# Kernel optimization log

Hardware: AMD Instinct MI355X
Metric: run time of the kernel (lower is better)

Reference implementation:

```python
import jax, jax.numpy as jnp
import numpy as np

D_MODEL, D_HEAD, N_HEADS, N_KV_HEADS = 4096, 128, 32, 8
EPS = 1e-5
N = 2048


def rms_norm(x, w, eps):
    return x * jax.lax.rsqrt(jnp.mean(x * x, axis=-1, keepdims=True) + eps) * w


def rope_swap(x):
    # [x0, x1, x2, x3] -> [-x1, x0, -x3, x2]
    xp = x.reshape(x.shape[:-1] + (-1, 2))
    return jnp.stack([-xp[..., 1], xp[..., 0]], axis=-1).reshape(x.shape)


def rope_rotate(x, r_cos, r_sin):
    return x * r_cos + rope_swap(x) * r_sin


def setup_inputs() -> dict:
    key = jax.random.key(0)
    ks = jax.random.split(key, 8)
    sd = 1.0 / np.sqrt(D_MODEL)
    return {
        "x": jax.random.normal(ks[0], (N, D_MODEL), dtype=jnp.float32),
        "r_cos": jax.random.normal(ks[1], (N, D_HEAD), dtype=jnp.float32),
        "r_sin": jax.random.normal(ks[2], (N, D_HEAD), dtype=jnp.float32),
        "w_norm": jnp.ones((D_MODEL,), dtype=jnp.float32),
        "wq": jax.random.normal(ks[3], (D_MODEL, N_HEADS * D_HEAD), dtype=jnp.float32) * sd,
        "wk": jax.random.normal(ks[4], (D_MODEL, N_KV_HEADS * D_HEAD), dtype=jnp.float32) * sd,
        "wv": jax.random.normal(ks[5], (D_MODEL, N_KV_HEADS * D_HEAD), dtype=jnp.float32) * sd,
        "wo": jax.random.normal(ks[6], (D_MODEL, D_MODEL), dtype=jnp.float32) * sd,
    }


def reference(x, r_cos, r_sin, w_norm, wq, wk, wv, wo):
    n = x.shape[0]
    residual = x
    h = rms_norm(x, w_norm, EPS)

    # projections -> [n_heads, n, d_head]
    q = (h @ wq).reshape(n, N_HEADS, D_HEAD).transpose(1, 0, 2)
    k = (h @ wk).reshape(n, N_KV_HEADS, D_HEAD).transpose(1, 0, 2)
    v = (h @ wv).reshape(n, N_KV_HEADS, D_HEAD).transpose(1, 0, 2)

    # GQA: repeat kv heads
    reps = N_HEADS // N_KV_HEADS
    k = jnp.repeat(k, reps, axis=0)
    v = jnp.repeat(v, reps, axis=0)

    q = rope_rotate(q, r_cos, r_sin)
    k = rope_rotate(k, r_cos, r_sin)

    mask = jnp.where(
        jnp.tril(jnp.ones((n, n), dtype=bool)), 0.0, -jnp.inf
    ).astype(x.dtype)
    scores = jnp.einsum("hnd,hmd->hnm", q, k) / np.sqrt(D_HEAD).astype(np.float32) + mask
    a = jnp.einsum("hnm,hmd->hnd", jax.nn.softmax(scores, axis=-1), v)

    a = a.transpose(1, 0, 2).reshape(n, N_HEADS * D_HEAD)
    return residual + a @ wo
```

## Files before the change

kernel.cpp:

```cpp
#include <hip/hip_runtime.h>
#include <stdint.h>
#include <math.h>

#define TOK 2048
#define DMODEL 4096
#define QKV_LD 5120
#define KVB 64
#define PS_LD 72

typedef __attribute__((ext_vector_type(8))) short short8;
typedef __attribute__((ext_vector_type(4))) short short4v;
typedef __attribute__((ext_vector_type(8))) __bf16 bf16x8;
typedef __attribute__((ext_vector_type(4))) float f32x4;

__device__ __forceinline__ unsigned short f2bf(float f) {
  unsigned u = __float_as_uint(f);
  u += 0x7fffu + ((u >> 16) & 1u);
  return (unsigned short)(u >> 16);
}

__device__ __forceinline__ void gl16(const void* g, void* l) {
  __builtin_amdgcn_global_load_lds((__attribute__((address_space(1))) void*)g,
                                   (__attribute__((address_space(3))) void*)l,
                                   16, 0, 0);
}

__device__ __forceinline__ f32x4 mfma16(short8 a, short8 b, f32x4 c) {
  return __builtin_amdgcn_mfma_f32_16x16x32_bf16(__builtin_bit_cast(bf16x8, a),
                                                 __builtin_bit_cast(bf16x8, b),
                                                 c, 0, 0, 0);
}

__device__ __forceinline__ float fexp2(float x) {
  float r;
  asm("v_exp_f32 %0, %1" : "=v"(r) : "v"(x));
  return r;
}

__global__ __launch_bounds__(256) void k_rmsnorm(const float* __restrict__ x,
                                                 const float* __restrict__ w,
                                                 unsigned short* __restrict__ h) {
  const int row = blockIdx.x;
  const float* xr = x + (size_t)row * DMODEL;
  float4 v[4];
  float ss = 0.f;
#pragma unroll
  for (int i = 0; i < 4; ++i) {
    v[i] = *(const float4*)(xr + threadIdx.x * 4 + i * 1024);
    ss += v[i].x * v[i].x + v[i].y * v[i].y + v[i].z * v[i].z + v[i].w * v[i].w;
  }
#pragma unroll
  for (int m = 1; m < 64; m <<= 1) ss += __shfl_xor(ss, m, 64);
  __shared__ float ws4[4];
  if ((threadIdx.x & 63) == 0) ws4[threadIdx.x >> 6] = ss;
  __syncthreads();
  const float scale = rsqrtf((ws4[0] + ws4[1] + ws4[2] + ws4[3]) * (1.0f / DMODEL) + 1e-5f);
  unsigned short* hr = h + (size_t)row * DMODEL;
#pragma unroll
  for (int i = 0; i < 4; ++i) {
    int col = threadIdx.x * 4 + i * 1024;
    float4 wv = *(const float4*)(w + col);
    uint2 o;
    o.x = (unsigned)f2bf(v[i].x * scale * wv.x) | ((unsigned)f2bf(v[i].y * scale * wv.y) << 16);
    o.y = (unsigned)f2bf(v[i].z * scale * wv.z) | ((unsigned)f2bf(v[i].w * scale * wv.w) << 16);
    *(uint2*)(hr + col) = o;
  }
}

__global__ __launch_bounds__(256) void k_wconvert(const float* __restrict__ W,
                                                  unsigned short* __restrict__ WT,
                                                  int K, int N) {
  __shared__ unsigned short tile[64][65];
  const int n0 = blockIdx.x * 64, k0 = blockIdx.y * 64;
  const int t = threadIdx.x;
  {
    const int r = t >> 2, c0 = (t & 3) * 16;
    const float* src = W + (size_t)(k0 + r) * N + n0 + c0;
#pragma unroll
    for (int i = 0; i < 4; ++i) {
      float4 f = *(const float4*)(src + i * 4);
      tile[r][c0 + i * 4 + 0] = f2bf(f.x);
      tile[r][c0 + i * 4 + 1] = f2bf(f.y);
      tile[r][c0 + i * 4 + 2] = f2bf(f.z);
      tile[r][c0 + i * 4 + 3] = f2bf(f.w);
    }
  }
  __syncthreads();
  {
    const int n = t >> 2, c0 = (t & 3) * 16;
    unsigned short* dst = WT + (size_t)(n0 + n) * K + k0 + c0;
    unsigned short v[16];
#pragma unroll
    for (int i = 0; i < 16; ++i) v[i] = tile[c0 + i][n];
    uint4 o0, o1;
    o0.x = v[0] | ((unsigned)v[1] << 16);  o0.y = v[2] | ((unsigned)v[3] << 16);
    o0.z = v[4] | ((unsigned)v[5] << 16);  o0.w = v[6] | ((unsigned)v[7] << 16);
    o1.x = v[8] | ((unsigned)v[9] << 16);  o1.y = v[10] | ((unsigned)v[11] << 16);
    o1.z = v[12] | ((unsigned)v[13] << 16); o1.w = v[14] | ((unsigned)v[15] << 16);
    *(uint4*)dst = o0;
    *(uint4*)(dst + 8) = o1;
  }
}

__device__ __forceinline__ short8 rdfrag(const unsigned short* buf, int row, int kc) {
  return *(const short8*)((const char*)buf + row * 128 + ((kc ^ (row & 7)) << 4));
}

template <int BM, int BN, int HALF>
__device__ __forceinline__ void stage_half(const unsigned short* __restrict__ A,
                                           const unsigned short* __restrict__ BT,
                                           unsigned short* __restrict__ buf,
                                           int m0, int n0, int K, int kt, int tid) {
  constexpr int AL = BM / 64, BL = BN / 64;
  constexpr int A0 = HALF ? AL / 2 : 0, A1 = HALF ? AL : AL / 2;
  constexpr int B0 = HALF ? BL / 2 : 0, B1 = HALF ? BL : BL / 2;
  unsigned short* bbuf = buf + BM * 64;
#pragma unroll
  for (int i = A0; i < A1; ++i) {
    const int s = i * 512 + tid, row = s >> 3, ch = s & 7;
    gl16(A + (size_t)(m0 + row) * K + kt + ((ch ^ (row & 7)) << 3), (char*)buf + s * 16);
  }
#pragma unroll
  for (int i = B0; i < B1; ++i) {
    const int s = i * 512 + tid, row = s >> 3, ch = s & 7;
    gl16(BT + (size_t)(n0 + row) * K + kt + ((ch ^ (row & 7)) << 3), (char*)bbuf + s * 16);
  }
}

template <int BM, int BN, int MODE>
__global__ __launch_bounds__(512, 2) void k_gemm_big(const unsigned short* __restrict__ A,
                                                     const unsigned short* __restrict__ BT,
                                                     const float* __restrict__ resid,
                                                     void* __restrict__ Cout,
                                                     unsigned short* __restrict__ vtg,
                                                     int M, int N, int K) {
  extern __shared__ __align__(16) unsigned short lds[];
  constexpr int MREP = BM / 32;
  constexpr int NREP = BN / 64;
  constexpr int TILE = (BM + BN) * 64;

  const int tid = threadIdx.x, lane = tid & 63;
  const int w = tid >> 6, wm = w >> 2, wn = w & 3;
  const int lr = lane & 15, lh = lane >> 4;

  const int wg0 = blockIdx.x;
  const int xcd = wg0 & 7, l = wg0 >> 3;
  const int m0 = (((xcd >> 2) << 2) + (l >> 3)) * BM;
  const int n0 = (((xcd & 3) << 3) + (l & 7)) * BN;

  const f32x4 zf = {0.f, 0.f, 0.f, 0.f};
  f32x4 acc[MREP][NREP];
#pragma unroll
  for (int i = 0; i < MREP; ++i) {
#pragma unroll
    for (int j = 0; j < NREP; ++j) acc[i][j] = zf;
  }

  const int arow0 = wm * (BM / 2);
  const int brow0 = wn * (BN / 4);
  const int NT = K >> 6;
  int cur = 0;

  stage_half<BM, BN, 0>(A, BT, lds, m0, n0, K, 0, tid);
  stage_half<BM, BN, 1>(A, BT, lds, m0, n0, K, 0, tid);
  __syncthreads();

  for (int t = 0; t < NT; ++t) {
    const unsigned short* abuf = lds + cur * TILE;
    const unsigned short* bbuf = abuf + BM * 64;
    unsigned short* nbuf = lds + (cur ^ 1) * TILE;
    const bool pre = (t + 1 < NT);
    const int ktn = (t + 1) << 6;

    short8 bfr[NREP][2];
#pragma unroll
    for (int nr = 0; nr < NREP; ++nr) {
#pragma unroll
      for (int kk = 0; kk < 2; ++kk)
        bfr[nr][kk] = rdfrag(bbuf, brow0 + nr * 16 + lr, kk * 4 + lh);
    }

#pragma unroll
    for (int p = 0; p < 4; ++p) {
      short8 afr[2][2];
#pragma unroll
      for (int mi = 0; mi < 2; ++mi) {
#pragma unroll
        for (int kk = 0; kk < 2; ++kk)
          afr[mi][kk] = rdfrag(abuf, arow0 + (p * 2 + mi) * 16 + lr, kk * 4 + lh);
      }
      if (p == 0 && pre) stage_half<BM, BN, 0>(A, BT, nbuf, m0, n0, K, ktn, tid);
      if (p == 1 && pre) stage_half<BM, BN, 1>(A, BT, nbuf, m0, n0, K, ktn, tid);
      __builtin_amdgcn_s_barrier();
      __builtin_amdgcn_s_setprio(1);
#pragma unroll
      for (int mi = 0; mi < 2; ++mi) {
#pragma unroll
        for (int nr = 0; nr < NREP; ++nr) {
#pragma unroll
          for (int kk = 0; kk < 2; ++kk)
            acc[p * 2 + mi][nr] = mfma16(afr[mi][kk], bfr[nr][kk], acc[p * 2 + mi][nr]);
        }
      }
      __builtin_amdgcn_s_setprio(0);
      if (p < 3) __builtin_amdgcn_s_barrier();
    }
    __syncthreads();
    cur ^= 1;
  }

#pragma unroll
  for (int ai = 0; ai < MREP; ++ai) {
#pragma unroll
    for (int ni = 0; ni < NREP; ++ni) {
      const int colg = n0 + wn * (BN / 4) + ni * 16 + lr;
      const int rowg0 = m0 + wm * (BM / 2) + ai * 16 + 4 * lh;
      if (MODE == 1) {
#pragma unroll
        for (int r = 0; r < 4; ++r)
          ((float*)Cout)[(size_t)(rowg0 + r) * N + colg] =
              acc[ai][ni][r] + resid[(size_t)(rowg0 + r) * N + colg];
      } else if (colg >= 5120) {
        short4v o;
#pragma unroll
        for (int r = 0; r < 4; ++r) o[r] = (short)f2bf(acc[ai][ni][r]);
        *(short4v*)(vtg + (size_t)(colg - 5120) * TOK + rowg0) = o;
      } else {
#pragma unroll
        for (int r = 0; r < 4; ++r)
          ((unsigned short*)Cout)[(size_t)(rowg0 + r) * QKV_LD + colg] = f2bf(acc[ai][ni][r]);
      }
    }
  }
}

__global__ __launch_bounds__(256) void k_rope(unsigned short* __restrict__ qkv,
                                              const float* __restrict__ rc,
                                              const float* __restrict__ rs) {
  const int row = blockIdx.y;
  const int p = blockIdx.x * 256 + threadIdx.x;
  const int col = p * 2;
  const int d = col & 127;
  unsigned short* ptr = qkv + (size_t)row * QKV_LD + col;
  const unsigned both = *(const unsigned*)ptr;
  const float x0 = __uint_as_float((both & 0xffffu) << 16);
  const float x1 = __uint_as_float(both & 0xffff0000u);
  const float c0 = rc[row * 128 + d], c1 = rc[row * 128 + d + 1];
  const float s0 = rs[row * 128 + d], s1 = rs[row * 128 + d + 1];
  const float y0 = x0 * c0 - x1 * s0;
  const float y1 = x1 * c1 + x0 * s1;
  *(unsigned*)ptr = (unsigned)f2bf(y0) | ((unsigned)f2bf(y1) << 16);
}

__global__ __launch_bounds__(256) void k_attn(const unsigned short* __restrict__ qkv,
                                              const unsigned short* __restrict__ vtg,
                                              unsigned short* __restrict__ aout) {
  __shared__ __align__(16) unsigned short Ks[KVB * 128];
  __shared__ __align__(16) unsigned short Vt[128 * KVB];
  __shared__ __align__(16) unsigned short Ps[4][16 * PS_LD];
  const int head = blockIdx.y;
  const int hkv = head >> 2;
  const int tid = threadIdx.x, lane = tid & 63, w = tid >> 6;
  const int lr = lane & 15, lh = lane >> 4;
  const float scale2 = 0.08838834764831845f * 1.44269504088896340736f;
  const f32x4 zf = {0.f, 0.f, 0.f, 0.f};

  for (int half = 0; half < 2; ++half) {
    const int qt = half ? (31 - blockIdx.x) : blockIdx.x;
    const int q0 = qt * 64;

    short8 qf[4];
    {
      const unsigned short* qbase = qkv + (size_t)(q0 + w * 16 + lr) * QKV_LD + head * 128;
#pragma unroll
      for (int kd = 0; kd < 4; ++kd) qf[kd] = *(const short8*)(qbase + kd * 32 + lh * 8);
    }
    f32x4 oacc[8];
#pragma unroll
    for (int vt = 0; vt < 8; ++vt) oacc[vt] = zf;
    float Mr[4], Lr[4];
#pragma unroll
    for (int r = 0; r < 4; ++r) { Mr[r] = -INFINITY; Lr[r] = 0.f; }

    const int nt = qt + 1;
    for (int t = 0; t < nt; ++t) {
      const int kv0 = t * KVB;
      __syncthreads();
#pragma unroll
      for (int c = 0; c < 4; ++c) {
        const int s = c * 256 + w * 64 + lane;
        const int row = s >> 4, cp = s & 15;
        gl16(qkv + (size_t)(kv0 + row) * QKV_LD + 4096 + hkv * 128 + ((cp ^ (row & 7)) * 8),
             (char*)Ks + (c * 256 + w * 64) * 16);
      }
#pragma unroll
      for (int c = 0; c < 4; ++c) {
        const int s = c * 256 + w * 64 + lane;
        const int row = s >> 3, cp = s & 7;
        gl16(vtg + (size_t)(hkv * 128 + row) * TOK + kv0 + ((cp ^ (row & 7)) * 8),
             (char*)Vt + (c * 256 + w * 64) * 16);
      }
      __syncthreads();

      f32x4 sacc[4];
#pragma unroll
      for (int ct = 0; ct < 4; ++ct) {
        sacc[ct] = zf;
        const int row = ct * 16 + lr;
#pragma unroll
        for (int kd = 0; kd < 4; ++kd) {
          const short8 kf = *(const short8*)((const char*)Ks + row * 256 +
                                             (((kd * 4 + lh) ^ (row & 7)) * 16));
          sacc[ct] = mfma16(qf[kd], kf, sacc[ct]);
        }
      }

      float scv[4], pv[4][4];
#pragma unroll
      for (int r = 0; r < 4; ++r) {
        const int qrow = q0 + w * 16 + 4 * lh + r;
        float s0 = sacc[0][r] * scale2;
        float s1 = sacc[1][r] * scale2;
        float s2 = sacc[2][r] * scale2;
        float s3 = sacc[3][r] * scale2;
        if (kv0 + lr > qrow) s0 = -INFINITY;
        if (kv0 + 16 + lr > qrow) s1 = -INFINITY;
        if (kv0 + 32 + lr > qrow) s2 = -INFINITY;
        if (kv0 + 48 + lr > qrow) s3 = -INFINITY;
        float tmax = fmaxf(fmaxf(s0, s1), fmaxf(s2, s3));
        tmax = fmaxf(tmax, __shfl_xor(tmax, 1, 16));
        tmax = fmaxf(tmax, __shfl_xor(tmax, 2, 16));
        tmax = fmaxf(tmax, __shfl_xor(tmax, 4, 16));
        tmax = fmaxf(tmax, __shfl_xor(tmax, 8, 16));
        const float mnew = fmaxf(Mr[r], tmax);
        const float sc = fexp2(Mr[r] - mnew);
        Mr[r] = mnew;
        const float p0 = fexp2(s0 - mnew);
        const float p1 = fexp2(s1 - mnew);
        const float p2 = fexp2(s2 - mnew);
        const float p3 = fexp2(s3 - mnew);
        float ps = (p0 + p1) + (p2 + p3);
        ps += __shfl_xor(ps, 1, 16);
        ps += __shfl_xor(ps, 2, 16);
        ps += __shfl_xor(ps, 4, 16);
        ps += __shfl_xor(ps, 8, 16);
        Lr[r] = Lr[r] * sc + ps;
        scv[r] = sc;
        pv[r][0] = p0; pv[r][1] = p1; pv[r][2] = p2; pv[r][3] = p3;
      }
#pragma unroll
      for (int vt = 0; vt < 8; ++vt) {
#pragma unroll
        for (int r = 0; r < 4; ++r) oacc[vt][r] *= scv[r];
      }

      unsigned short* pw = Ps[w];
#pragma unroll
      for (int r = 0; r < 4; ++r) {
#pragma unroll
        for (int ct = 0; ct < 4; ++ct)
          pw[(4 * lh + r) * PS_LD + ct * 16 + lr] = f2bf(pv[r][ct]);
      }
      asm volatile("s_waitcnt lgkmcnt(0)" ::: "memory");
      short8 pf[2];
      pf[0] = *(const short8*)(pw + lr * PS_LD + lh * 8);
      pf[1] = *(const short8*)(pw + lr * PS_LD + 32 + lh * 8);
      __builtin_amdgcn_s_setprio(1);
#pragma unroll
      for (int vt = 0; vt < 8; ++vt) {
        const int d = vt * 16 + lr;
#pragma unroll
        for (int kb = 0; kb < 2; ++kb) {
          const short8 vf = *(const short8*)((const char*)Vt + d * 128 +
                                             (((kb * 4 + lh) ^ (lr & 7)) * 16));
          oacc[vt] = mfma16(pf[kb], vf, oacc[vt]);
        }
      }
      __builtin_amdgcn_s_setprio(0);
    }

#pragma unroll
    for (int r = 0; r < 4; ++r) {
      const float inv = 1.0f / Lr[r];
      const size_t rowoff = (size_t)(q0 + w * 16 + 4 * lh + r) * DMODEL + head * 128;
#pragma unroll
      for (int vt = 0; vt < 8; ++vt)
        aout[rowoff + vt * 16 + lr] = f2bf(oacc[vt][r] * inv);
    }
  }
}

extern "C" void kernel_launch(void* const* d_in, const int* in_sizes, int n_in,
                              void* d_out, int out_size, void* d_ws, size_t ws_size,
                              hipStream_t stream) {
  (void)in_sizes; (void)n_in; (void)out_size; (void)ws_size;
  const float* x     = (const float*)d_in[0];
  const float* r_cos = (const float*)d_in[1];
  const float* r_sin = (const float*)d_in[2];
  const float* wnorm = (const float*)d_in[3];
  const float* wq    = (const float*)d_in[4];
  const float* wk    = (const float*)d_in[5];
  const float* wv    = (const float*)d_in[6];
  const float* wo    = (const float*)d_in[7];

  unsigned short* bufA = (unsigned short*)d_ws;
  unsigned short* qkvb = bufA + (size_t)TOK * DMODEL;
  unsigned short* wT   = qkvb + (size_t)TOK * QKV_LD;
  unsigned short* vtg  = wT + (size_t)6144 * DMODEL;

  hipFuncSetAttribute((const void*)k_gemm_big<256, 192, 0>,
                      hipFuncAttributeMaxDynamicSharedMemorySize, 4 * (256 + 192) * 64);
  hipFuncSetAttribute((const void*)k_gemm_big<256, 128, 1>,
                      hipFuncAttributeMaxDynamicSharedMemorySize, 4 * (256 + 128) * 64);

  k_rmsnorm<<<TOK, 256, 0, stream>>>(x, wnorm, bufA);
  k_wconvert<<<dim3(64, 64), 256, 0, stream>>>(wq, wT, DMODEL, 4096);
  k_wconvert<<<dim3(16, 64), 256, 0, stream>>>(wk, wT + (size_t)4096 * DMODEL, DMODEL, 1024);
  k_wconvert<<<dim3(16, 64), 256, 0, stream>>>(wv, wT + (size_t)5120 * DMODEL, DMODEL, 1024);
  k_gemm_big<256, 192, 0><<<dim3(256), 512, 4 * (256 + 192) * 64, stream>>>(
      bufA, wT, nullptr, qkvb, vtg, TOK, 6144, DMODEL);
  k_wconvert<<<dim3(64, 64), 256, 0, stream>>>(wo, wT, DMODEL, 4096);
  k_rope<<<dim3(10, TOK), 256, 0, stream>>>(qkvb, r_cos, r_sin);
  k_attn<<<dim3(16, 32), 256, 0, stream>>>(qkvb, vtg, bufA);
  k_gemm_big<256, 128, 1><<<dim3(256), 512, 4 * (256 + 128) * 64, stream>>>(
      bufA, wT, x, d_out, nullptr, TOK, DMODEL, DMODEL);
}
```

Baseline: 334.7 us.

## Fuse RoPE into QKV GEMM epilogue, restructure GEMM pipeline, double-buffer attention KV

Three changes at once. The RoPE rotation moves into the QKV GEMM epilogue, using a lane shuffle to fetch the pair partner, so the separate rope kernel and its extra pass over qkv disappear. The GEMM main loop is reorganised around explicit vmcnt waits and fewer barriers, with the next tile's second half prefetched between MFMA phases. The attention kernel gets double-buffered K/V tiles in dynamic LDS so the next tile's loads overlap compute. This adds more LDS use and relies on hand-counted waitcnt values that must match the number of outstanding loads.

Result: faster. 325.8 us (-2.7%).

```diff
diff --git a/kernel.cpp b/kernel.cpp
--- a/kernel.cpp
+++ b/kernel.cpp
@@ -35,6 +35,15 @@
   float r;
   asm("v_exp_f32 %0, %1" : "=v"(r) : "v"(x));
   return r;
+}
+
+template <int N>
+__device__ __forceinline__ void waitvm() {
+  if constexpr (N == 0) asm volatile("s_waitcnt vmcnt(0)" ::: "memory");
+  else if constexpr (N == 3) asm volatile("s_waitcnt vmcnt(3)" ::: "memory");
+  else if constexpr (N == 4) asm volatile("s_waitcnt vmcnt(4)" ::: "memory");
+  else if constexpr (N == 8) asm volatile("s_waitcnt vmcnt(8)" ::: "memory");
+  else static_assert(N == 0 || N == 3 || N == 4 || N == 8, "add literal");
 }
 
 __global__ __launch_bounds__(256) void k_rmsnorm(const float* __restrict__ x,
@@ -111,9 +120,10 @@
                                            const unsigned short* __restrict__ BT,
                                            unsigned short* __restrict__ buf,
                                            int m0, int n0, int K, int kt, int tid) {
-  constexpr int AL = BM / 64, BL = BN / 64;
-  constexpr int A0 = HALF ? AL / 2 : 0, A1 = HALF ? AL : AL / 2;
-  constexpr int B0 = HALF ? BL / 2 : 0, B1 = HALF ? BL : BL / 2;
+  constexpr int LA = BM / 64, LB = BN / 64;
+  constexpr int H0A = LA / 2, H0B = (LB + 1) / 2;
+  constexpr int A0 = HALF ? H0A : 0, A1 = HALF ? LA : H0A;
+  constexpr int B0 = HALF ? H0B : 0, B1 = HALF ? LB : H0B;
   unsigned short* bbuf = buf + BM * 64;
 #pragma unroll
   for (int i = A0; i < A1; ++i) {
@@ -133,11 +143,15 @@
                                                      const float* __restrict__ resid,
                                                      void* __restrict__ Cout,
                                                      unsigned short* __restrict__ vtg,
+                                                     const float* __restrict__ rc,
+                                                     const float* __restrict__ rs,
                                                      int M, int N, int K) {
   extern __shared__ __align__(16) unsigned short lds[];
   constexpr int MREP = BM / 32;
   constexpr int NREP = BN / 64;
   constexpr int TILE = (BM + BN) * 64;
+  constexpr int LA = BM / 64, LB = BN / 64;
+  constexpr int H0 = LA / 2 + (LB + 1) / 2;
 
   const int tid = threadIdx.x, lane = tid & 63;
   const int w = tid >> 6, wm = w >> 2, wn = w & 3;
@@ -163,7 +177,6 @@
 
   stage_half<BM, BN, 0>(A, BT, lds, m0, n0, K, 0, tid);
   stage_half<BM, BN, 1>(A, BT, lds, m0, n0, K, 0, tid);
-  __syncthreads();
 
   for (int t = 0; t < NT; ++t) {
     const unsigned short* abuf = lds + cur * TILE;
@@ -172,40 +185,61 @@
     const bool pre = (t + 1 < NT);
     const int ktn = (t + 1) << 6;
 
-    short8 bfr[NREP][2];
-#pragma unroll
-    for (int nr = 0; nr < NREP; ++nr) {
-#pragma unroll
-      for (int kk = 0; kk < 2; ++kk)
-        bfr[nr][kk] = rdfrag(bbuf, brow0 + nr * 16 + lr, kk * 4 + lh);
-    }
-
-#pragma unroll
-    for (int p = 0; p < 4; ++p) {
-      short8 afr[2][2];
-#pragma unroll
-      for (int mi = 0; mi < 2; ++mi) {
-#pragma unroll
-        for (int kk = 0; kk < 2; ++kk)
-          afr[mi][kk] = rdfrag(abuf, arow0 + (p * 2 + mi) * 16 + lr, kk * 4 + lh);
-      }
-      if (p == 0 && pre) stage_half<BM, BN, 0>(A, BT, nbuf, m0, n0, K, ktn, tid);
-      if (p == 1 && pre) stage_half<BM, BN, 1>(A, BT, nbuf, m0, n0, K, ktn, tid);
-      __builtin_amdgcn_s_barrier();
-      __builtin_amdgcn_s_setprio(1);
-#pragma unroll
-      for (int mi = 0; mi < 2; ++mi) {
-#pragma unroll
-        for (int nr = 0; nr < NREP; ++nr) {
-#pragma unroll
-          for (int kk = 0; kk < 2; ++kk)
-            acc[p * 2 + mi][nr] = mfma16(afr[mi][kk], bfr[nr][kk], acc[p * 2 + mi][nr]);
-        }
-      }
-      __builtin_amdgcn_s_setprio(0);
-      if (p < 3) __builtin_amdgcn_s_barrier();
-    }
-    __syncthreads();
+    short8 bfr[NREP], afr[4];
+    if (pre) {
+      stage_half<BM, BN, 0>(A, BT, nbuf, m0, n0, K, ktn, tid);
+      waitvm<H0>();
+    } else {
+      waitvm<0>();
+    }
+    __builtin_amdgcn_s_barrier();
+#pragma unroll
+    for (int nr = 0; nr < NREP; ++nr) bfr[nr] = rdfrag(bbuf, brow0 + nr * 16 + lr, lh);
+#pragma unroll
+    for (int mi = 0; mi < 4; ++mi) afr[mi] = rdfrag(abuf, arow0 + mi * 16 + lr, lh);
+    __builtin_amdgcn_s_setprio(1);
+#pragma unroll
+    for (int mi = 0; mi < 4; ++mi) {
+#pragma unroll
+      for (int nr = 0; nr < NREP; ++nr)
+        acc[mi][nr] = mfma16(afr[mi], bfr[nr], acc[mi][nr]);
+    }
+    __builtin_amdgcn_s_setprio(0);
+    if (pre) stage_half<BM, BN, 1>(A, BT, nbuf, m0, n0, K, ktn, tid);
+#pragma unroll
+    for (int mi = 0; mi < 4; ++mi) afr[mi] = rdfrag(abuf, arow0 + (4 + mi) * 16 + lr, lh);
+    __builtin_amdgcn_s_setprio(1);
+#pragma unroll
+    for (int mi = 0; mi < 4; ++mi) {
+#pragma unroll
+      for (int nr = 0; nr < NREP; ++nr)
+        acc[4 + mi][nr] = mfma16(afr[mi], bfr[nr], acc[4 + mi][nr]);
+    }
+    __builtin_amdgcn_s_setprio(0);
+#pragma unroll
+    for (int nr = 0; nr < NREP; ++nr) bfr[nr] = rdfrag(bbuf, brow0 + nr * 16 + lr, 4 + lh);
+#pragma unroll
+    for (int mi = 0; mi < 4; ++mi) afr[mi] = rdfrag(abuf, arow0 + mi * 16 + lr, 4 + lh);
+    __builtin_amdgcn_s_setprio(1);
+#pragma unroll
+    for (int mi = 0; mi < 4; ++mi) {
+#pragma unroll
+      for (int nr = 0; nr < NREP; ++nr)
+        acc[mi][nr] = mfma16(afr[mi], bfr[nr], acc[mi][nr]);
+    }
+    __builtin_amdgcn_s_setprio(0);
+#pragma unroll
+    for (int mi = 0; mi < 4; ++mi) afr[mi] = rdfrag(abuf, arow0 + (4 + mi) * 16 + lr, 4 + lh);
+    asm volatile("s_waitcnt lgkmcnt(0)" ::: "memory");
+    __builtin_amdgcn_s_barrier();
+    __builtin_amdgcn_s_setprio(1);
+#pragma unroll
+    for (int mi = 0; mi < 4; ++mi) {
+#pragma unroll
+      for (int nr = 0; nr < NREP; ++nr)
+        acc[4 + mi][nr] = mfma16(afr[mi], bfr[nr], acc[4 + mi][nr]);
+    }
+    __builtin_amdgcn_s_setprio(0);
     cur ^= 1;
   }
 
@@ -226,38 +260,29 @@
         for (int r = 0; r < 4; ++r) o[r] = (short)f2bf(acc[ai][ni][r]);
         *(short4v*)(vtg + (size_t)(colg - 5120) * TOK + rowg0) = o;
       } else {
-#pragma unroll
-        for (int r = 0; r < 4; ++r)
-          ((unsigned short*)Cout)[(size_t)(rowg0 + r) * QKV_LD + colg] = f2bf(acc[ai][ni][r]);
-      }
-    }
-  }
-}
-
-__global__ __launch_bounds__(256) void k_rope(unsigned short* __restrict__ qkv,
-                                              const float* __restrict__ rc,
-                                              const float* __restrict__ rs) {
-  const int row = blockIdx.y;
-  const int p = blockIdx.x * 256 + threadIdx.x;
-  const int col = p * 2;
-  const int d = col & 127;
-  unsigned short* ptr = qkv + (size_t)row * QKV_LD + col;
-  const unsigned both = *(const unsigned*)ptr;
-  const float x0 = __uint_as_float((both & 0xffffu) << 16);
-  const float x1 = __uint_as_float(both & 0xffff0000u);
-  const float c0 = rc[row * 128 + d], c1 = rc[row * 128 + d + 1];
-  const float s0 = rs[row * 128 + d], s1 = rs[row * 128 + d + 1];
-  const float y0 = x0 * c0 - x1 * s0;
-  const float y1 = x1 * c1 + x0 * s1;
-  *(unsigned*)ptr = (unsigned)f2bf(y0) | ((unsigned)f2bf(y1) << 16);
+        const int d = colg & 127;
+#pragma unroll
+        for (int r = 0; r < 4; ++r) {
+          const int row = rowg0 + r;
+          const float v = acc[ai][ni][r];
+          const float p = __shfl_xor(v, 1, 64);
+          const float c = rc[row * 128 + d];
+          const float s = rs[row * 128 + d];
+          const float y = (lr & 1) ? fmaf(p, s, v * c) : fmaf(-p, s, v * c);
+          ((unsigned short*)Cout)[(size_t)row * QKV_LD + colg] = f2bf(y);
+        }
+      }
+    }
+  }
 }
 
 __global__ __launch_bounds__(256) void k_attn(const unsigned short* __restrict__ qkv,
                                               const unsigned short* __restrict__ vtg,
                                               unsigned short* __restrict__ aout) {
-  __shared__ __align__(16) unsigned short Ks[KVB * 128];
-  __shared__ __align__(16) unsigned short Vt[128 * KVB];
-  __shared__ __align__(16) unsigned short Ps[4][16 * PS_LD];
+  extern __shared__ __align__(16) unsigned short sm[];
+  unsigned short* const KsB = sm;
+  unsigned short* const VtB = sm + 2 * KVB * 128;
+  unsigned short* const Ps = sm + 4 * KVB * 128;
   const int head = blockIdx.y;
   const int hkv = head >> 2;
   const int tid = threadIdx.x, lane = tid & 63, w = tid >> 6;
@@ -283,24 +308,52 @@
     for (int r = 0; r < 4; ++r) { Mr[r] = -INFINITY; Lr[r] = 0.f; }
 
     const int nt = qt + 1;
-    for (int t = 0; t < nt; ++t) {
-      const int kv0 = t * KVB;
-      __syncthreads();
+    int cur = 0;
+
+    {
 #pragma unroll
       for (int c = 0; c < 4; ++c) {
         const int s = c * 256 + w * 64 + lane;
         const int row = s >> 4, cp = s & 15;
-        gl16(qkv + (size_t)(kv0 + row) * QKV_LD + 4096 + hkv * 128 + ((cp ^ (row & 7)) * 8),
-             (char*)Ks + (c * 256 + w * 64) * 16);
+        gl16(qkv + (size_t)row * QKV_LD + 4096 + hkv * 128 + ((cp ^ (row & 7)) * 8),
+             (char*)KsB + (c * 256 + w * 64) * 16);
       }
 #pragma unroll
       for (int c = 0; c < 4; ++c) {
         const int s = c * 256 + w * 64 + lane;
         const int row = s >> 3, cp = s & 7;
-        gl16(vtg + (size_t)(hkv * 128 + row) * TOK + kv0 + ((cp ^ (row & 7)) * 8),
-             (char*)Vt + (c * 256 + w * 64) * 16);
-      }
-      __syncthreads();
+        gl16(vtg + (size_t)(hkv * 128 + row) * TOK + ((cp ^ (row & 7)) * 8),
+             (char*)VtB + (c * 256 + w * 64) * 16);
+      }
+    }
+
+    for (int t = 0; t < nt; ++t) {
+      const unsigned short* Ks = KsB + cur * (KVB * 128);
+      const unsigned short* Vt = VtB + cur * (128 * KVB);
+      const int kv0 = t * KVB;
+      if (t + 1 < nt) {
+        unsigned short* Ksn = KsB + (cur ^ 1) * (KVB * 128);
+        unsigned short* Vtn = VtB + (cur ^ 1) * (128 * KVB);
+        const int kvn = (t + 1) * KVB;
+#pragma unroll
+        for (int c = 0; c < 4; ++c) {
+          const int s = c * 256 + w * 64 + lane;
+          const int row = s >> 4, cp = s & 15;
+          gl16(qkv + (size_t)(kvn + row) * QKV_LD + 4096 + hkv * 128 + ((cp ^ (row & 7)) * 8),
+               (char*)Ksn + (c * 256 + w * 64) * 16);
+        }
+#pragma unroll
+        for (int c = 0; c < 4; ++c) {
+          const int s = c * 256 + w * 64 + lane;
+          const int row = s >> 3, cp = s & 7;
+          gl16(vtg + (size_t)(hkv * 128 + row) * TOK + kvn + ((cp ^ (row & 7)) * 8),
+               (char*)Vtn + (c * 256 + w * 64) * 16);
+        }
+        waitvm<8>();
+      } else {
+        waitvm<0>();
+      }
+      __builtin_amdgcn_s_barrier();
 
       f32x4 sacc[4];
 #pragma unroll
@@ -354,7 +407,7 @@
         for (int r = 0; r < 4; ++r) oacc[vt][r] *= scv[r];
       }
 
-      unsigned short* pw = Ps[w];
+      unsigned short* pw = Ps + w * (16 * PS_LD);
 #pragma unroll
       for (int r = 0; r < 4; ++r) {
 #pragma unroll
@@ -377,6 +430,9 @@
         }
       }
       __builtin_amdgcn_s_setprio(0);
+      asm volatile("s_waitcnt lgkmcnt(0)" ::: "memory");
+      __builtin_amdgcn_s_barrier();
+      cur ^= 1;
     }
 
 #pragma unroll
@@ -412,16 +468,18 @@
                       hipFuncAttributeMaxDynamicSharedMemorySize, 4 * (256 + 192) * 64);
   hipFuncSetAttribute((const void*)k_gemm_big<256, 128, 1>,
                       hipFuncAttributeMaxDynamicSharedMemorySize, 4 * (256 + 128) * 64);
+  const int attn_lds = 4 * KVB * 128 * 2 + 4 * 16 * PS_LD * 2;
+  hipFuncSetAttribute((const void*)k_attn,
+                      hipFuncAttributeMaxDynamicSharedMemorySize, attn_lds);
 
   k_rmsnorm<<<TOK, 256, 0, stream>>>(x, wnorm, bufA);
   k_wconvert<<<dim3(64, 64), 256, 0, stream>>>(wq, wT, DMODEL, 4096);
   k_wconvert<<<dim3(16, 64), 256, 0, stream>>>(wk, wT + (size_t)4096 * DMODEL, DMODEL, 1024);
   k_wconvert<<<dim3(16, 64), 256, 0, stream>>>(wv, wT + (size_t)5120 * DMODEL, DMODEL, 1024);
   k_gemm_big<256, 192, 0><<<dim3(256), 512, 4 * (256 + 192) * 64, stream>>>(
-      bufA, wT, nullptr, qkvb, vtg, TOK, 6144, DMODEL);
+      bufA, wT, nullptr, qkvb, vtg, r_cos, r_sin, TOK, 6144, DMODEL);
   k_wconvert<<<dim3(64, 64), 256, 0, stream>>>(wo, wT, DMODEL, 4096);
-  k_rope<<<dim3(10, TOK), 256, 0, stream>>>(qkvb, r_cos, r_sin);
-  k_attn<<<dim3(16, 32), 256, 0, stream>>>(qkvb, vtg, bufA);
+  k_attn<<<dim3(16, 32), 256, attn_lds, stream>>>(qkvb, vtg, bufA);
   k_gemm_big<256, 128, 1><<<dim3(256), 512, 4 * (256 + 128) * 64, stream>>>(
-      bufA, wT, x, d_out, nullptr, TOK, DMODEL, DMODEL);
-}
+      bufA, wT, x, d_out, nullptr, nullptr, nullptr, TOK, DMODEL, DMODEL);
+}
```
